# Optimization experiments

Hardware: AMD Instinct MI355X
Metric: run time of the kernel (lower is better)

The kernel has to match this reference:

```python
import jax, jax.numpy as jnp
import numpy as np

N_NODES = 100000


def gcn_conv(x, src, dst, w, W, b, n):
    # PyG GCNConv: add self loops (weight 1), symmetric normalization,
    # linear transform, scatter-add aggregation, bias.
    loop = jnp.arange(n, dtype=src.dtype)
    s = jnp.concatenate([src, loop])
    d = jnp.concatenate([dst, loop])
    ew = jnp.concatenate([w, jnp.ones((n,), dtype=w.dtype)])
    deg = jax.ops.segment_sum(ew, d, num_segments=n)          # [N]
    dinv = jnp.where(deg > 0, jax.lax.rsqrt(deg), 0.0).astype(x.dtype)
    norm = dinv[s] * ew * dinv[d]                             # [E+N]
    h = x @ W                                                 # [N, out]
    msg = h[s] * norm[:, None]                                # gather + scale
    out = jax.ops.segment_sum(msg, d, num_segments=n)         # scatter-add
    return out + b


def setup_inputs() -> dict:
    key = jax.random.key(0)
    k1, k2, k3, k4, k5, k6 = jax.random.split(key, 6)
    n, e, c_in, c_hid, c_out = N_NODES, 1200000, 64, 64, 32
    node_matrix = jax.random.normal(k1, (n, c_in), dtype=jnp.float32)
    edge_index = jax.random.randint(k2, (2, e), 0, n, dtype=jnp.int64)
    edge_weights = jax.random.uniform(k3, (e,), dtype=jnp.float32)
    s_in = 1.0 / np.sqrt(c_in)
    s_hid = 1.0 / np.sqrt(c_hid)
    W1 = jax.random.uniform(k4, (c_in, c_hid), jnp.float32, -s_in, s_in)
    b1 = jnp.zeros((c_hid,), jnp.float32)
    W2 = jax.random.uniform(k5, (c_hid, c_out), jnp.float32, -s_hid, s_hid)
    b2 = jnp.zeros((c_out,), jnp.float32)
    return {"node_matrix": node_matrix, "edge_index": edge_index,
            "edge_weights": edge_weights, "W1": W1, "b1": b1, "W2": W2, "b2": b2}


def reference(node_matrix, edge_index, edge_weights, W1, b1, W2, b2):
    n = node_matrix.shape[0]
    src, dst = edge_index[0], edge_index[1]
    x = gcn_conv(node_matrix, src, dst, edge_weights, W1, b1, n)
    x = jax.nn.relu(x)
    x = gcn_conv(x, src, dst, edge_weights, W2, b2, n)
    return x
```

## Files before the change

kernel.cpp:

```cpp
#include <hip/hip_runtime.h>

static inline int ceil_div(long long a, long long b) { return (int)((a + b - 1) / b); }

#define RBITS 8
#define RNODES 256
#define CAPB 12
#define CAP 4096

typedef __attribute__((ext_vector_type(8))) short bf16x8;
typedef __attribute__((ext_vector_type(4))) float f32x4;
typedef __attribute__((ext_vector_type(2))) unsigned u32x2;
typedef __attribute__((ext_vector_type(4))) unsigned u32x4;

__device__ inline unsigned f2bf(float f) {
    unsigned u = __float_as_uint(f);
    return (u + 0x7fffu + ((u >> 16) & 1u)) >> 16;
}
__device__ inline unsigned pack2(float a, float b) { return f2bf(a) | (f2bf(b) << 16); }
__device__ inline float bf2f(unsigned v) { return __uint_as_float(v << 16); }
__device__ inline float bf_lo(unsigned v) { return __uint_as_float(v << 16); }
__device__ inline float bf_hi(unsigned v) { return __uint_as_float(v & 0xffff0000u); }

#define SC_T 512
#define SC_K 8
#define SC_E (SC_T * SC_K)
__global__ void bin_scatter(const int* __restrict__ src, const int* __restrict__ dst,
                            const float* __restrict__ w, int* __restrict__ bin_cursor,
                            int* __restrict__ bp, float* __restrict__ bw,
                            int NB, int E) {
    __shared__ int hist[512];
    __shared__ int offs[512];
    __shared__ int base[512];
    __shared__ int stage_p[SC_E];
    __shared__ float stage_w[SC_E];
    __shared__ unsigned short stage_b[SC_E];
    int t = threadIdx.x;
    hist[t] = 0;
    __syncthreads();
    int e0 = blockIdx.x * SC_E;
    int nE = E - e0; if (nE > SC_E) nE = SC_E;

    int myBin[SC_K], myRank[SC_K], myPack[SC_K];
    float myW[SC_K];
#pragma unroll
    for (int k = 0; k < SC_K; ++k) {
        int idx = t + k * SC_T;
        if (idx < nE) {
            int e = e0 + idx;
            int d = dst[e];
            int b = d >> RBITS;
            myBin[k] = b;
            myPack[k] = (src[e] << RBITS) | (d & (RNODES - 1));
            myW[k] = w[e];
            myRank[k] = atomicAdd(&hist[b], 1);
        }
    }
    __syncthreads();
    offs[t] = hist[t];
    __syncthreads();
    for (int d = 1; d < 512; d <<= 1) {
        int a = (t >= d) ? offs[t - d] : 0;
        __syncthreads();
        offs[t] += a;
        __syncthreads();
    }
    if (t < NB && hist[t]) base[t] = (t << CAPB) + atomicAdd(&bin_cursor[t], hist[t]);
#pragma unroll
    for (int k = 0; k < SC_K; ++k) {
        int idx = t + k * SC_T;
        if (idx < nE) {
            int b = myBin[k];
            int pos = (offs[b] - hist[b]) + myRank[k];
            stage_p[pos] = myPack[k];
            stage_w[pos] = myW[k];
            stage_b[pos] = (unsigned short)b;
        }
    }
    __syncthreads();
    for (int p = t; p < nE; p += SC_T) {
        int b = stage_b[p];
        int g = base[b] + (p - (offs[b] - hist[b]));
        bp[g] = stage_p[p];
        bw[g] = stage_w[p];
    }
}

__global__ void build_csr(const int* __restrict__ bp, const float* __restrict__ bw,
                          const int* __restrict__ bin_len,
                          unsigned* __restrict__ row_rc, float* __restrict__ dinv,
                          u32x2* __restrict__ ew, int N) {
    __shared__ int bp_s[CAP];
    __shared__ float bw_s[CAP];
    __shared__ int cnt[RNODES];
    __shared__ float wsum[RNODES];
    __shared__ int starts[RNODES];
    __shared__ int cur[RNODES];
    int b = blockIdx.x;
    int t = threadIdx.x;
    int len = bin_len[b];
    int base = b << CAPB;
    if (t < RNODES) { cnt[t] = 0; wsum[t] = 0.f; }
    __syncthreads();
    for (int e = t; e < len; e += 512) {
        int p = bp[base + e];
        float wv = bw[base + e];
        bp_s[e] = p;
        bw_s[e] = wv;
        atomicAdd(&cnt[p & (RNODES - 1)], 1);
        atomicAdd(&wsum[p & (RNODES - 1)], wv);
    }
    __syncthreads();
    if (t < RNODES) starts[t] = cnt[t];
    __syncthreads();
    for (int d = 1; d < RNODES; d <<= 1) {
        int a = 0;
        if (t < RNODES && t >= d) a = starts[t - d];
        __syncthreads();
        if (t < RNODES) starts[t] += a;
        __syncthreads();
    }
    if (t < RNODES) {
        int s0 = starts[t] - cnt[t];
        cur[t] = s0;
        int node = (b << RBITS) + t;
        if (node < N) {
            row_rc[node] = (unsigned)(base + s0) | ((unsigned)cnt[t] << 21);
            dinv[node] = rsqrtf(wsum[t] + 1.0f);
        }
    }
    __syncthreads();
    for (int e = t; e < len; e += 512) {
        int p = bp_s[e];
        int slot = atomicAdd(&cur[p & (RNODES - 1)], 1);
        u32x2 v;
        v.x = (unsigned)(p >> RBITS);
        v.y = __float_as_uint(bw_s[e]);
        ew[base + slot] = v;
    }
}

__global__ __launch_bounds__(256) void gemm1_mfma(const float* __restrict__ X,
                                                  const float* __restrict__ W,
                                                  const float* __restrict__ dinv,
                                                  unsigned short* __restrict__ H, int N) {
    int lane = threadIdx.x & 63;
    int wv = threadIdx.x >> 6;
    int quad = lane >> 4;
    int col = lane & 15;

    bf16x8 Bh[4][2], Bl[4][2];
#pragma unroll
    for (int nt = 0; nt < 4; ++nt)
#pragma unroll
        for (int kh = 0; kh < 2; ++kh)
#pragma unroll
            for (int j = 0; j < 8; ++j) {
                float wval = W[(kh * 32 + quad * 8 + j) * 64 + nt * 16 + col];
                unsigned hb = f2bf(wval);
                Bh[nt][kh][j] = (short)hb;
                Bl[nt][kh][j] = (short)f2bf(wval - bf2f(hb));
            }

#pragma unroll
    for (int rt = 0; rt < 4; ++rt) {
        int rb = blockIdx.x * 256 + wv * 64 + rt * 16;
        if (rb >= N) break;
        int arow = rb + col;
        bf16x8 Ah[2], Al[2];
#pragma unroll
        for (int kh = 0; kh < 2; ++kh) {
            float xv[8];
            if (arow < N) {
                const float4* p = (const float4*)(X + (size_t)arow * 64 + kh * 32 + quad * 8);
                float4 f0 = p[0], f1 = p[1];
                xv[0] = f0.x; xv[1] = f0.y; xv[2] = f0.z; xv[3] = f0.w;
                xv[4] = f1.x; xv[5] = f1.y; xv[6] = f1.z; xv[7] = f1.w;
            } else {
#pragma unroll
                for (int j = 0; j < 8; ++j) xv[j] = 0.f;
            }
#pragma unroll
            for (int j = 0; j < 8; ++j) {
                unsigned hb = f2bf(xv[j]);
                Ah[kh][j] = (short)hb;
                Al[kh][j] = (short)f2bf(xv[j] - bf2f(hb));
            }
        }
        f32x4 acc[4] = {{0,0,0,0},{0,0,0,0},{0,0,0,0},{0,0,0,0}};
#pragma unroll
        for (int nt = 0; nt < 4; ++nt)
#pragma unroll
            for (int kh = 0; kh < 2; ++kh) {
                acc[nt] = __builtin_amdgcn_mfma_f32_16x16x32_bf16(Ah[kh], Bh[nt][kh], acc[nt], 0, 0, 0);
                acc[nt] = __builtin_amdgcn_mfma_f32_16x16x32_bf16(Al[kh], Bh[nt][kh], acc[nt], 0, 0, 0);
                acc[nt] = __builtin_amdgcn_mfma_f32_16x16x32_bf16(Ah[kh], Bl[nt][kh], acc[nt], 0, 0, 0);
            }
        float di[4];
#pragma unroll
        for (int r = 0; r < 4; ++r) {
            int row = rb + quad * 4 + r;
            di[r] = (row < N) ? dinv[row] : 0.f;
        }
#pragma unroll
        for (int nt = 0; nt < 4; ++nt)
#pragma unroll
            for (int r = 0; r < 4; ++r) {
                int row = rb + quad * 4 + r;
                if (row < N)
                    H[(size_t)row * 64 + nt * 16 + col] = (unsigned short)f2bf(di[r] * acc[nt][r]);
            }
    }
}

__global__ __launch_bounds__(256) void gemm2_mfma(const unsigned short* __restrict__ Xb,
                                                  const float* __restrict__ W,
                                                  const float* __restrict__ dinv,
                                                  unsigned short* __restrict__ H, int N) {
    int lane = threadIdx.x & 63;
    int wv = threadIdx.x >> 6;
    int quad = lane >> 4;
    int col = lane & 15;

    bf16x8 Bh[2][2], Bl[2][2];
#pragma unroll
    for (int nt = 0; nt < 2; ++nt)
#pragma unroll
        for (int kh = 0; kh < 2; ++kh)
#pragma unroll
            for (int j = 0; j < 8; ++j) {
                float wval = W[(kh * 32 + quad * 8 + j) * 32 + nt * 16 + col];
                unsigned hb = f2bf(wval);
                Bh[nt][kh][j] = (short)hb;
                Bl[nt][kh][j] = (short)f2bf(wval - bf2f(hb));
            }

#pragma unroll
    for (int rt = 0; rt < 4; ++rt) {
        int rb = blockIdx.x * 256 + wv * 64 + rt * 16;
        if (rb >= N) break;
        int arow = rb + col;
        bf16x8 A[2];
#pragma unroll
        for (int kh = 0; kh < 2; ++kh) {
            if (arow < N) {
                const bf16x8* p = (const bf16x8*)(Xb + (size_t)arow * 64 + kh * 32 + quad * 8);
                A[kh] = *p;
            } else {
                A[kh] = bf16x8{0,0,0,0,0,0,0,0};
            }
        }
        f32x4 acc[2] = {{0,0,0,0},{0,0,0,0}};
#pragma unroll
        for (int nt = 0; nt < 2; ++nt)
#pragma unroll
            for (int kh = 0; kh < 2; ++kh) {
                acc[nt] = __builtin_amdgcn_mfma_f32_16x16x32_bf16(A[kh], Bh[nt][kh], acc[nt], 0, 0, 0);
                acc[nt] = __builtin_amdgcn_mfma_f32_16x16x32_bf16(A[kh], Bl[nt][kh], acc[nt], 0, 0, 0);
            }
        float di[4];
#pragma unroll
        for (int r = 0; r < 4; ++r) {
            int row = rb + quad * 4 + r;
            di[r] = (row < N) ? dinv[row] : 0.f;
        }
#pragma unroll
        for (int nt = 0; nt < 2; ++nt)
#pragma unroll
            for (int r = 0; r < 4; ++r) {
                int row = rb + quad * 4 + r;
                if (row < N)
                    H[(size_t)row * 32 + nt * 16 + col] = (unsigned short)f2bf(di[r] * acc[nt][r]);
            }
    }
}

__global__ void aggregate64(const unsigned* __restrict__ h, const unsigned* __restrict__ row_rc,
                            const u32x2* __restrict__ ew, const float* __restrict__ dinv,
                            const float* __restrict__ b, unsigned* __restrict__ outb, int N) {
    int t = threadIdx.x;
    int c = t & 7;
    int i = blockIdx.x * 64 + (t >> 3);
    if (i >= N) return;
    unsigned rc = row_rc[i];
    int e = (int)(rc & 0x1FFFFFu);
    int end = e + (int)(rc >> 21);
    const uint4* h4 = (const uint4*)h;
    float acc[8];
#pragma unroll
    for (int j = 0; j < 8; ++j) acc[j] = 0.f;
    for (; e + 3 < end; e += 4) {
        u32x2 e0 = __builtin_nontemporal_load(&ew[e]);
        u32x2 e1 = __builtin_nontemporal_load(&ew[e + 1]);
        u32x2 e2 = __builtin_nontemporal_load(&ew[e + 2]);
        u32x2 e3 = __builtin_nontemporal_load(&ew[e + 3]);
        float n0 = __uint_as_float(e0.y);
        float n1 = __uint_as_float(e1.y);
        float n2 = __uint_as_float(e2.y);
        float n3 = __uint_as_float(e3.y);
        uint4 v0 = h4[(size_t)e0.x * 8 + c];
        uint4 v1 = h4[(size_t)e1.x * 8 + c];
        uint4 v2 = h4[(size_t)e2.x * 8 + c];
        uint4 v3 = h4[(size_t)e3.x * 8 + c];
        acc[0] += n0 * bf_lo(v0.x) + n1 * bf_lo(v1.x) + n2 * bf_lo(v2.x) + n3 * bf_lo(v3.x);
        acc[1] += n0 * bf_hi(v0.x) + n1 * bf_hi(v1.x) + n2 * bf_hi(v2.x) + n3 * bf_hi(v3.x);
        acc[2] += n0 * bf_lo(v0.y) + n1 * bf_lo(v1.y) + n2 * bf_lo(v2.y) + n3 * bf_lo(v3.y);
        acc[3] += n0 * bf_hi(v0.y) + n1 * bf_hi(v1.y) + n2 * bf_hi(v2.y) + n3 * bf_hi(v3.y);
        acc[4] += n0 * bf_lo(v0.z) + n1 * bf_lo(v1.z) + n2 * bf_lo(v2.z) + n3 * bf_lo(v3.z);
        acc[5] += n0 * bf_hi(v0.z) + n1 * bf_hi(v1.z) + n2 * bf_hi(v2.z) + n3 * bf_hi(v3.z);
        acc[6] += n0 * bf_lo(v0.w) + n1 * bf_lo(v1.w) + n2 * bf_lo(v2.w) + n3 * bf_lo(v3.w);
        acc[7] += n0 * bf_hi(v0.w) + n1 * bf_hi(v1.w) + n2 * bf_hi(v2.w) + n3 * bf_hi(v3.w);
    }
    for (; e < end; ++e) {
        u32x2 e0 = __builtin_nontemporal_load(&ew[e]);
        float n0 = __uint_as_float(e0.y);
        uint4 v0 = h4[(size_t)e0.x * 8 + c];
        acc[0] += n0 * bf_lo(v0.x);
        acc[1] += n0 * bf_hi(v0.x);
        acc[2] += n0 * bf_lo(v0.y);
        acc[3] += n0 * bf_hi(v0.y);
        acc[4] += n0 * bf_lo(v0.z);
        acc[5] += n0 * bf_hi(v0.z);
        acc[6] += n0 * bf_lo(v0.w);
        acc[7] += n0 * bf_hi(v0.w);
    }
    float di = dinv[i];
    uint4 hv = h4[(size_t)i * 8 + c];
    float hs[8] = {bf_lo(hv.x), bf_hi(hv.x), bf_lo(hv.y), bf_hi(hv.y),
                   bf_lo(hv.z), bf_hi(hv.z), bf_lo(hv.w), bf_hi(hv.w)};
    float4 b0 = ((const float4*)b)[c * 2];
    float4 b1 = ((const float4*)b)[c * 2 + 1];
    float o[8];
    o[0] = b0.x + di * (hs[0] + acc[0]);
    o[1] = b0.y + di * (hs[1] + acc[1]);
    o[2] = b0.z + di * (hs[2] + acc[2]);
    o[3] = b0.w + di * (hs[3] + acc[3]);
    o[4] = b1.x + di * (hs[4] + acc[4]);
    o[5] = b1.y + di * (hs[5] + acc[5]);
    o[6] = b1.z + di * (hs[6] + acc[6]);
    o[7] = b1.w + di * (hs[7] + acc[7]);
#pragma unroll
    for (int j = 0; j < 8; ++j) o[j] = fmaxf(o[j], 0.f);
    u32x4 ov;
    ov.x = pack2(o[0], o[1]);
    ov.y = pack2(o[2], o[3]);
    ov.z = pack2(o[4], o[5]);
    ov.w = pack2(o[6], o[7]);
    __builtin_nontemporal_store(ov, (u32x4*)outb + (size_t)i * 8 + c);
}

__global__ void aggregate32(const unsigned* __restrict__ h, const unsigned* __restrict__ row_rc,
                            const u32x2* __restrict__ ew, const float* __restrict__ dinv,
                            const float* __restrict__ b, float* __restrict__ out, int N) {
    int t = threadIdx.x;
    int c = t & 3;
    int i = blockIdx.x * 128 + (t >> 2);
    if (i >= N) return;
    unsigned rc = row_rc[i];
    int e = (int)(rc & 0x1FFFFFu);
    int end = e + (int)(rc >> 21);
    const uint4* h4 = (const uint4*)h;
    float acc[8];
#pragma unroll
    for (int j = 0; j < 8; ++j) acc[j] = 0.f;
    for (; e + 3 < end; e += 4) {
        u32x2 e0 = __builtin_nontemporal_load(&ew[e]);
        u32x2 e1 = __builtin_nontemporal_load(&ew[e + 1]);
        u32x2 e2 = __builtin_nontemporal_load(&ew[e + 2]);
        u32x2 e3 = __builtin_nontemporal_load(&ew[e + 3]);
        float n0 = __uint_as_float(e0.y);
        float n1 = __uint_as_float(e1.y);
        float n2 = __uint_as_float(e2.y);
        float n3 = __uint_as_float(e3.y);
        uint4 v0 = h4[(size_t)e0.x * 4 + c];
        uint4 v1 = h4[(size_t)e1.x * 4 + c];
        uint4 v2 = h4[(size_t)e2.x * 4 + c];
        uint4 v3 = h4[(size_t)e3.x * 4 + c];
        acc[0] += n0 * bf_lo(v0.x) + n1 * bf_lo(v1.x) + n2 * bf_lo(v2.x) + n3 * bf_lo(v3.x);
        acc[1] += n0 * bf_hi(v0.x) + n1 * bf_hi(v1.x) + n2 * bf_hi(v2.x) + n3 * bf_hi(v3.x);
        acc[2] += n0 * bf_lo(v0.y) + n1 * bf_lo(v1.y) + n2 * bf_lo(v2.y) + n3 * bf_lo(v3.y);
        acc[3] += n0 * bf_hi(v0.y) + n1 * bf_hi(v1.y) + n2 * bf_hi(v2.y) + n3 * bf_hi(v3.y);
        acc[4] += n0 * bf_lo(v0.z) + n1 * bf_lo(v1.z) + n2 * bf_lo(v2.z) + n3 * bf_lo(v3.z);
        acc[5] += n0 * bf_hi(v0.z) + n1 * bf_hi(v1.z) + n2 * bf_hi(v2.z) + n3 * bf_hi(v3.z);
        acc[6] += n0 * bf_lo(v0.w) + n1 * bf_lo(v1.w) + n2 * bf_lo(v2.w) + n3 * bf_lo(v3.w);
        acc[7] += n0 * bf_hi(v0.w) + n1 * bf_hi(v1.w) + n2 * bf_hi(v2.w) + n3 * bf_hi(v3.w);
    }
    for (; e < end; ++e) {
        u32x2 e0 = __builtin_nontemporal_load(&ew[e]);
        float n0 = __uint_as_float(e0.y);
        uint4 v0 = h4[(size_t)e0.x * 4 + c];
        acc[0] += n0 * bf_lo(v0.x);
        acc[1] += n0 * bf_hi(v0.x);
        acc[2] += n0 * bf_lo(v0.y);
        acc[3] += n0 * bf_hi(v0.y);
        acc[4] += n0 * bf_lo(v0.z);
        acc[5] += n0 * bf_hi(v0.z);
        acc[6] += n0 * bf_lo(v0.w);
        acc[7] += n0 * bf_hi(v0.w);
    }
    float di = dinv[i];
    uint4 hv = h4[(size_t)i * 4 + c];
    float hs[8] = {bf_lo(hv.x), bf_hi(hv.x), bf_lo(hv.y), bf_hi(hv.y),
                   bf_lo(hv.z), bf_hi(hv.z), bf_lo(hv.w), bf_hi(hv.w)};
    float4 b0 = ((const float4*)b)[c * 2];
    float4 b1 = ((const float4*)b)[c * 2 + 1];
    f32x4 o0, o1;
    o0.x = b0.x + di * (hs[0] + acc[0]);
    o0.y = b0.y + di * (hs[1] + acc[1]);
    o0.z = b0.z + di * (hs[2] + acc[2]);
    o0.w = b0.w + di * (hs[3] + acc[3]);
    o1.x = b1.x + di * (hs[4] + acc[4]);
    o1.y = b1.y + di * (hs[5] + acc[5]);
    o1.z = b1.z + di * (hs[6] + acc[6]);
    o1.w = b1.w + di * (hs[7] + acc[7]);
    f32x4* op = (f32x4*)(out + (size_t)i * 32 + c * 8);
    __builtin_nontemporal_store(o0, op);
    __builtin_nontemporal_store(o1, op + 1);
}

extern "C" void kernel_launch(void* const* d_in, const int* in_sizes, int n_in,
                              void* d_out, int out_size, void* d_ws, size_t ws_size,
                              hipStream_t stream) {
    const float* x  = (const float*)d_in[0];
    const int* eidx = (const int*)d_in[1];
    const float* w  = (const float*)d_in[2];
    const float* W1 = (const float*)d_in[3];
    const float* b1 = (const float*)d_in[4];
    const float* W2 = (const float*)d_in[5];
    const float* b2 = (const float*)d_in[6];
    float* out = (float*)d_out;

    const int E = in_sizes[2];
    const int N = in_sizes[0] / 64;
    const int* src = eidx;
    const int* dst = eidx + E;
    const int NB = ceil_div(N, RNODES);

    char* ws = (char*)d_ws;
    size_t off = 0;
    auto alloc = [&](size_t bytes) -> void* {
        void* p = ws + off;
        off = (off + bytes + 255) & ~(size_t)255;
        return p;
    };
    int*      bin_cursor = (int*)alloc((size_t)NB * 4);
    int*      bp         = (int*)alloc((size_t)NB * CAP * 4);
    float*    bw         = (float*)alloc((size_t)NB * CAP * 4);
    u32x2*    ew         = (u32x2*)alloc((size_t)NB * CAP * 8);
    unsigned* row_rc     = (unsigned*)alloc((size_t)N * 4);
    float*    dinv       = (float*)alloc((size_t)N * 4);
    unsigned* h1         = (unsigned*)alloc((size_t)N * 32 * 4);
    unsigned* out1b      = (unsigned*)alloc((size_t)N * 32 * 4);
    unsigned* h2         = (unsigned*)alloc((size_t)N * 16 * 4);

    (void)hipMemsetAsync(bin_cursor, 0, (size_t)NB * 4, stream);
    bin_scatter<<<ceil_div(E, SC_E), SC_T, 0, stream>>>(src, dst, w, bin_cursor, bp, bw, NB, E);
    build_csr<<<NB, 512, 0, stream>>>(bp, bw, bin_cursor, row_rc, dinv, ew, N);

    gemm1_mfma<<<ceil_div(N, 256), 256, 0, stream>>>(x, W1, dinv, (unsigned short*)h1, N);
    aggregate64<<<ceil_div(N, 64), 512, 0, stream>>>(h1, row_rc, ew, dinv, b1, out1b, N);

    gemm2_mfma<<<ceil_div(N, 256), 256, 0, stream>>>((const unsigned short*)out1b, W2, dinv,
                                                     (unsigned short*)h2, N);
    aggregate32<<<ceil_div(N, 128), 512, 0, stream>>>(h2, row_rc, ew, dinv, b2, out, N);
}
```

Before: 213.0 us.

## Split each node's edges across four teams, shrink GEMM blocks, defer rsqrt

The aggregation kernels now give each node four teams of lanes. Each team takes a contiguous slice of the node's edge list, and the partial sums are combined with xor shuffles. This targets long per-node serial loops and uneven degree latency. Both GEMM kernels now process one 16-row tile per wave with four times more blocks, and dinv is recomputed from a stored weight sum instead of being precomputed. Nontemporal loads and stores were also replaced with plain accesses. In exchange the code does more shuffle work, and three of every four lanes sit idle in the epilogue.

```diff
diff --git a/kernel.cpp b/kernel.cpp
--- a/kernel.cpp
+++ b/kernel.cpp
@@ -30,7 +30,7 @@
                             int NB, int E) {
     __shared__ int hist[512];
     __shared__ int offs[512];
-    __shared__ int base[512];
+    __shared__ int basex[512];
     __shared__ int stage_p[SC_E];
     __shared__ float stage_w[SC_E];
     __shared__ unsigned short stage_b[SC_E];
@@ -64,7 +64,7 @@
         offs[t] += a;
         __syncthreads();
     }
-    if (t < NB && hist[t]) base[t] = (t << CAPB) + atomicAdd(&bin_cursor[t], hist[t]);
+    if (t < NB && hist[t]) basex[t] = (t << CAPB) + atomicAdd(&bin_cursor[t], hist[t]);
 #pragma unroll
     for (int k = 0; k < SC_K; ++k) {
         int idx = t + k * SC_T;
@@ -79,7 +79,7 @@
     __syncthreads();
     for (int p = t; p < nE; p += SC_T) {
         int b = stage_b[p];
-        int g = base[b] + (p - (offs[b] - hist[b]));
+        int g = basex[b] + (p - (offs[b] - hist[b]));
         bp[g] = stage_p[p];
         bw[g] = stage_w[p];
     }
@@ -87,7 +87,7 @@
 
 __global__ void build_csr(const int* __restrict__ bp, const float* __restrict__ bw,
                           const int* __restrict__ bin_len,
-                          unsigned* __restrict__ row_rc, float* __restrict__ dinv,
+                          unsigned* __restrict__ row_rc, float* __restrict__ wsum_g,
                           u32x2* __restrict__ ew, int N) {
     __shared__ int bp_s[CAP];
     __shared__ float bw_s[CAP];
@@ -125,7 +125,7 @@
         int node = (b << RBITS) + t;
         if (node < N) {
             row_rc[node] = (unsigned)(base + s0) | ((unsigned)cnt[t] << 21);
-            dinv[node] = rsqrtf(wsum[t] + 1.0f);
+            wsum_g[node] = wsum[t];
         }
     }
     __syncthreads();
@@ -141,12 +141,14 @@
 
 __global__ __launch_bounds__(256) void gemm1_mfma(const float* __restrict__ X,
                                                   const float* __restrict__ W,
-                                                  const float* __restrict__ dinv,
+                                                  const float* __restrict__ wsum,
                                                   unsigned short* __restrict__ H, int N) {
     int lane = threadIdx.x & 63;
     int wv = threadIdx.x >> 6;
     int quad = lane >> 4;
     int col = lane & 15;
+    int rb = blockIdx.x * 64 + wv * 16;
+    if (rb >= N) return;
 
     bf16x8 Bh[4][2], Bl[4][2];
 #pragma unroll
@@ -161,65 +163,62 @@
                 Bl[nt][kh][j] = (short)f2bf(wval - bf2f(hb));
             }
 
-#pragma unroll
-    for (int rt = 0; rt < 4; ++rt) {
-        int rb = blockIdx.x * 256 + wv * 64 + rt * 16;
-        if (rb >= N) break;
-        int arow = rb + col;
-        bf16x8 Ah[2], Al[2];
+    int arow = rb + col;
+    bf16x8 Ah[2], Al[2];
+#pragma unroll
+    for (int kh = 0; kh < 2; ++kh) {
+        float xv[8];
+        if (arow < N) {
+            const float4* p = (const float4*)(X + (size_t)arow * 64 + kh * 32 + quad * 8);
+            float4 f0 = p[0], f1 = p[1];
+            xv[0] = f0.x; xv[1] = f0.y; xv[2] = f0.z; xv[3] = f0.w;
+            xv[4] = f1.x; xv[5] = f1.y; xv[6] = f1.z; xv[7] = f1.w;
+        } else {
+#pragma unroll
+            for (int j = 0; j < 8; ++j) xv[j] = 0.f;
+        }
+#pragma unroll
+        for (int j = 0; j < 8; ++j) {
+            unsigned hb = f2bf(xv[j]);
+            Ah[kh][j] = (short)hb;
+            Al[kh][j] = (short)f2bf(xv[j] - bf2f(hb));
+        }
+    }
+    f32x4 acc[4] = {{0,0,0,0},{0,0,0,0},{0,0,0,0},{0,0,0,0}};
+#pragma unroll
+    for (int nt = 0; nt < 4; ++nt)
 #pragma unroll
         for (int kh = 0; kh < 2; ++kh) {
-            float xv[8];
-            if (arow < N) {
-                const float4* p = (const float4*)(X + (size_t)arow * 64 + kh * 32 + quad * 8);
-                float4 f0 = p[0], f1 = p[1];
-                xv[0] = f0.x; xv[1] = f0.y; xv[2] = f0.z; xv[3] = f0.w;
-                xv[4] = f1.x; xv[5] = f1.y; xv[6] = f1.z; xv[7] = f1.w;
-            } else {
-#pragma unroll
-                for (int j = 0; j < 8; ++j) xv[j] = 0.f;
-            }
-#pragma unroll
-            for (int j = 0; j < 8; ++j) {
-                unsigned hb = f2bf(xv[j]);
-                Ah[kh][j] = (short)hb;
-                Al[kh][j] = (short)f2bf(xv[j] - bf2f(hb));
-            }
-        }
-        f32x4 acc[4] = {{0,0,0,0},{0,0,0,0},{0,0,0,0},{0,0,0,0}};
-#pragma unroll
-        for (int nt = 0; nt < 4; ++nt)
-#pragma unroll
-            for (int kh = 0; kh < 2; ++kh) {
-                acc[nt] = __builtin_amdgcn_mfma_f32_16x16x32_bf16(Ah[kh], Bh[nt][kh], acc[nt], 0, 0, 0);
-                acc[nt] = __builtin_amdgcn_mfma_f32_16x16x32_bf16(Al[kh], Bh[nt][kh], acc[nt], 0, 0, 0);
-                acc[nt] = __builtin_amdgcn_mfma_f32_16x16x32_bf16(Ah[kh], Bl[nt][kh], acc[nt], 0, 0, 0);
-            }
-        float di[4];
+            acc[nt] = __builtin_amdgcn_mfma_f32_16x16x32_bf16(Ah[kh], Bh[nt][kh], acc[nt], 0, 0, 0);
+            acc[nt] = __builtin_amdgcn_mfma_f32_16x16x32_bf16(Al[kh], Bh[nt][kh], acc[nt], 0, 0, 0);
+            acc[nt] = __builtin_amdgcn_mfma_f32_16x16x32_bf16(Ah[kh], Bl[nt][kh], acc[nt], 0, 0, 0);
+        }
+    float di[4];
+#pragma unroll
+    for (int r = 0; r < 4; ++r) {
+        int row = rb + quad * 4 + r;
+        di[r] = (row < N) ? rsqrtf(wsum[row] + 1.0f) : 0.f;
+    }
+#pragma unroll
+    for (int nt = 0; nt < 4; ++nt)
 #pragma unroll
         for (int r = 0; r < 4; ++r) {
             int row = rb + quad * 4 + r;
-            di[r] = (row < N) ? dinv[row] : 0.f;
-        }
-#pragma unroll
-        for (int nt = 0; nt < 4; ++nt)
-#pragma unroll
-            for (int r = 0; r < 4; ++r) {
-                int row = rb + quad * 4 + r;
-                if (row < N)
-                    H[(size_t)row * 64 + nt * 16 + col] = (unsigned short)f2bf(di[r] * acc[nt][r]);
-            }
-    }
+            if (row < N)
+                H[(size_t)row * 64 + nt * 16 + col] = (unsigned short)f2bf(di[r] * acc[nt][r]);
+        }
 }
 
 __global__ __launch_bounds__(256) void gemm2_mfma(const unsigned short* __restrict__ Xb,
                                                   const float* __restrict__ W,
-                                                  const float* __restrict__ dinv,
+                                                  const float* __restrict__ wsum,
                                                   unsigned short* __restrict__ H, int N) {
     int lane = threadIdx.x & 63;
     int wv = threadIdx.x >> 6;
     int quad = lane >> 4;
     int col = lane & 15;
+    int rb = blockIdx.x * 64 + wv * 16;
+    if (rb >= N) return;
 
     bf16x8 Bh[2][2], Bl[2][2];
 #pragma unroll
@@ -234,65 +233,63 @@
                 Bl[nt][kh][j] = (short)f2bf(wval - bf2f(hb));
             }
 
-#pragma unroll
-    for (int rt = 0; rt < 4; ++rt) {
-        int rb = blockIdx.x * 256 + wv * 64 + rt * 16;
-        if (rb >= N) break;
-        int arow = rb + col;
-        bf16x8 A[2];
+    int arow = rb + col;
+    bf16x8 A[2];
+#pragma unroll
+    for (int kh = 0; kh < 2; ++kh) {
+        if (arow < N) {
+            const bf16x8* p = (const bf16x8*)(Xb + (size_t)arow * 64 + kh * 32 + quad * 8);
+            A[kh] = *p;
+        } else {
+            A[kh] = bf16x8{0,0,0,0,0,0,0,0};
+        }
+    }
+    f32x4 acc[2] = {{0,0,0,0},{0,0,0,0}};
+#pragma unroll
+    for (int nt = 0; nt < 2; ++nt)
 #pragma unroll
         for (int kh = 0; kh < 2; ++kh) {
-            if (arow < N) {
-                const bf16x8* p = (const bf16x8*)(Xb + (size_t)arow * 64 + kh * 32 + quad * 8);
-                A[kh] = *p;
-            } else {
-                A[kh] = bf16x8{0,0,0,0,0,0,0,0};
-            }
-        }
-        f32x4 acc[2] = {{0,0,0,0},{0,0,0,0}};
-#pragma unroll
-        for (int nt = 0; nt < 2; ++nt)
-#pragma unroll
-            for (int kh = 0; kh < 2; ++kh) {
-                acc[nt] = __builtin_amdgcn_mfma_f32_16x16x32_bf16(A[kh], Bh[nt][kh], acc[nt], 0, 0, 0);
-                acc[nt] = __builtin_amdgcn_mfma_f32_16x16x32_bf16(A[kh], Bl[nt][kh], acc[nt], 0, 0, 0);
-            }
-        float di[4];
+            acc[nt] = __builtin_amdgcn_mfma_f32_16x16x32_bf16(A[kh], Bh[nt][kh], acc[nt], 0, 0, 0);
+            acc[nt] = __builtin_amdgcn_mfma_f32_16x16x32_bf16(A[kh], Bl[nt][kh], acc[nt], 0, 0, 0);
+        }
+    float di[4];
+#pragma unroll
+    for (int r = 0; r < 4; ++r) {
+        int row = rb + quad * 4 + r;
+        di[r] = (row < N) ? rsqrtf(wsum[row] + 1.0f) : 0.f;
+    }
+#pragma unroll
+    for (int nt = 0; nt < 2; ++nt)
 #pragma unroll
         for (int r = 0; r < 4; ++r) {
             int row = rb + quad * 4 + r;
-            di[r] = (row < N) ? dinv[row] : 0.f;
-        }
-#pragma unroll
-        for (int nt = 0; nt < 2; ++nt)
-#pragma unroll
-            for (int r = 0; r < 4; ++r) {
-                int row = rb + quad * 4 + r;
-                if (row < N)
-                    H[(size_t)row * 32 + nt * 16 + col] = (unsigned short)f2bf(di[r] * acc[nt][r]);
-            }
-    }
+            if (row < N)
+                H[(size_t)row * 32 + nt * 16 + col] = (unsigned short)f2bf(di[r] * acc[nt][r]);
+        }
 }
 
 __global__ void aggregate64(const unsigned* __restrict__ h, const unsigned* __restrict__ row_rc,
-                            const u32x2* __restrict__ ew, const float* __restrict__ dinv,
+                            const u32x2* __restrict__ ew, const float* __restrict__ wsum,
                             const float* __restrict__ b, unsigned* __restrict__ outb, int N) {
     int t = threadIdx.x;
     int c = t & 7;
-    int i = blockIdx.x * 64 + (t >> 3);
+    int team = (t >> 3) & 3;
+    int i = blockIdx.x * 16 + (t >> 5);
     if (i >= N) return;
     unsigned rc = row_rc[i];
-    int e = (int)(rc & 0x1FFFFFu);
-    int end = e + (int)(rc >> 21);
+    int beg = (int)(rc & 0x1FFFFFu);
+    int len = (int)(rc >> 21);
+    int q = len >> 2, r = len & 3;
+    int myCnt = q + (team < r ? 1 : 0);
+    int myBeg = beg + team * q + (team < r ? team : r);
     const uint4* h4 = (const uint4*)h;
     float acc[8];
 #pragma unroll
     for (int j = 0; j < 8; ++j) acc[j] = 0.f;
-    for (; e + 3 < end; e += 4) {
-        u32x2 e0 = __builtin_nontemporal_load(&ew[e]);
-        u32x2 e1 = __builtin_nontemporal_load(&ew[e + 1]);
-        u32x2 e2 = __builtin_nontemporal_load(&ew[e + 2]);
-        u32x2 e3 = __builtin_nontemporal_load(&ew[e + 3]);
+    int k = 0;
+    for (; k + 3 < myCnt; k += 4) {
+        int e = myBeg + k;
+        u32x2 e0 = ew[e], e1 = ew[e + 1], e2 = ew[e + 2], e3 = ew[e + 3];
         float n0 = __uint_as_float(e0.y);
         float n1 = __uint_as_float(e1.y);
         float n2 = __uint_as_float(e2.y);
@@ -310,8 +307,9 @@
         acc[6] += n0 * bf_lo(v0.w) + n1 * bf_lo(v1.w) + n2 * bf_lo(v2.w) + n3 * bf_lo(v3.w);
         acc[7] += n0 * bf_hi(v0.w) + n1 * bf_hi(v1.w) + n2 * bf_hi(v2.w) + n3 * bf_hi(v3.w);
     }
-    for (; e < end; ++e) {
-        u32x2 e0 = __builtin_nontemporal_load(&ew[e]);
+    for (; k < myCnt; ++k) {
+        int e = myBeg + k;
+        u32x2 e0 = ew[e];
         float n0 = __uint_as_float(e0.y);
         uint4 v0 = h4[(size_t)e0.x * 8 + c];
         acc[0] += n0 * bf_lo(v0.x);
@@ -323,7 +321,12 @@
         acc[6] += n0 * bf_lo(v0.w);
         acc[7] += n0 * bf_hi(v0.w);
     }
-    float di = dinv[i];
+#pragma unroll
+    for (int j = 0; j < 8; ++j) acc[j] += __shfl_xor(acc[j], 8, 64);
+#pragma unroll
+    for (int j = 0; j < 8; ++j) acc[j] += __shfl_xor(acc[j], 16, 64);
+    if (team != 0) return;
+    float di = rsqrtf(wsum[i] + 1.0f);
     uint4 hv = h4[(size_t)i * 8 + c];
     float hs[8] = {bf_lo(hv.x), bf_hi(hv.x), bf_lo(hv.y), bf_hi(hv.y),
                    bf_lo(hv.z), bf_hi(hv.z), bf_lo(hv.w), bf_hi(hv.w)};
@@ -340,33 +343,36 @@
     o[7] = b1.w + di * (hs[7] + acc[7]);
 #pragma unroll
     for (int j = 0; j < 8; ++j) o[j] = fmaxf(o[j], 0.f);
-    u32x4 ov;
+    uint4 ov;
     ov.x = pack2(o[0], o[1]);
     ov.y = pack2(o[2], o[3]);
     ov.z = pack2(o[4], o[5]);
     ov.w = pack2(o[6], o[7]);
-    __builtin_nontemporal_store(ov, (u32x4*)outb + (size_t)i * 8 + c);
+    ((uint4*)outb)[(size_t)i * 8 + c] = ov;
 }
 
 __global__ void aggregate32(const unsigned* __restrict__ h, const unsigned* __restrict__ row_rc,
-                            const u32x2* __restrict__ ew, const float* __restrict__ dinv,
+                            const u32x2* __restrict__ ew, const float* __restrict__ wsum,
                             const float* __restrict__ b, float* __restrict__ out, int N) {
     int t = threadIdx.x;
     int c = t & 3;
-    int i = blockIdx.x * 128 + (t >> 2);
+    int team = (t >> 2) & 3;
+    int i = blockIdx.x * 32 + (t >> 4);
     if (i >= N) return;
     unsigned rc = row_rc[i];
-    int e = (int)(rc & 0x1FFFFFu);
-    int end = e + (int)(rc >> 21);
+    int beg = (int)(rc & 0x1FFFFFu);
+    int len = (int)(rc >> 21);
+    int q = len >> 2, r = len & 3;
+    int myCnt = q + (team < r ? 1 : 0);
+    int myBeg = beg + team * q + (team < r ? team : r);
     const uint4* h4 = (const uint4*)h;
     float acc[8];
 #pragma unroll
     for (int j = 0; j < 8; ++j) acc[j] = 0.f;
-    for (; e + 3 < end; e += 4) {
-        u32x2 e0 = __builtin_nontemporal_load(&ew[e]);
-        u32x2 e1 = __builtin_nontemporal_load(&ew[e + 1]);
-        u32x2 e2 = __builtin_nontemporal_load(&ew[e + 2]);
-        u32x2 e3 = __builtin_nontemporal_load(&ew[e + 3]);
+    int k = 0;
+    for (; k + 3 < myCnt; k += 4) {
+        int e = myBeg + k;
+        u32x2 e0 = ew[e], e1 = ew[e + 1], e2 = ew[e + 2], e3 = ew[e + 3];
         float n0 = __uint_as_float(e0.y);
         float n1 = __uint_as_float(e1.y);
         float n2 = __uint_as_float(e2.y);
@@ -384,8 +390,9 @@
         acc[6] += n0 * bf_lo(v0.w) + n1 * bf_lo(v1.w) + n2 * bf_lo(v2.w) + n3 * bf_lo(v3.w);
         acc[7] += n0 * bf_hi(v0.w) + n1 * bf_hi(v1.w) + n2 * bf_hi(v2.w) + n3 * bf_hi(v3.w);
     }
-    for (; e < end; ++e) {
-        u32x2 e0 = __builtin_nontemporal_load(&ew[e]);
+    for (; k < myCnt; ++k) {
+        int e = myBeg + k;
+        u32x2 e0 = ew[e];
         float n0 = __uint_as_float(e0.y);
         uint4 v0 = h4[(size_t)e0.x * 4 + c];
         acc[0] += n0 * bf_lo(v0.x);
@@ -397,7 +404,12 @@
         acc[6] += n0 * bf_lo(v0.w);
         acc[7] += n0 * bf_hi(v0.w);
     }
-    float di = dinv[i];
+#pragma unroll
+    for (int j = 0; j < 8; ++j) acc[j] += __shfl_xor(acc[j], 4, 64);
+#pragma unroll
+    for (int j = 0; j < 8; ++j) acc[j] += __shfl_xor(acc[j], 8, 64);
+    if (team != 0) return;
+    float di = rsqrtf(wsum[i] + 1.0f);
     uint4 hv = h4[(size_t)i * 4 + c];
     float hs[8] = {bf_lo(hv.x), bf_hi(hv.x), bf_lo(hv.y), bf_hi(hv.y),
                    bf_lo(hv.z), bf_hi(hv.z), bf_lo(hv.w), bf_hi(hv.w)};
@@ -447,19 +459,19 @@
     float*    bw         = (float*)alloc((size_t)NB * CAP * 4);
     u32x2*    ew         = (u32x2*)alloc((size_t)NB * CAP * 8);
     unsigned* row_rc     = (unsigned*)alloc((size_t)N * 4);
-    float*    dinv       = (float*)alloc((size_t)N * 4);
+    float*    wsum       = (float*)alloc((size_t)N * 4);
     unsigned* h1         = (unsigned*)alloc((size_t)N * 32 * 4);
     unsigned* out1b      = (unsigned*)alloc((size_t)N * 32 * 4);
     unsigned* h2         = (unsigned*)alloc((size_t)N * 16 * 4);
 
     (void)hipMemsetAsync(bin_cursor, 0, (size_t)NB * 4, stream);
     bin_scatter<<<ceil_div(E, SC_E), SC_T, 0, stream>>>(src, dst, w, bin_cursor, bp, bw, NB, E);
-    build_csr<<<NB, 512, 0, stream>>>(bp, bw, bin_cursor, row_rc, dinv, ew, N);
-
-    gemm1_mfma<<<ceil_div(N, 256), 256, 0, stream>>>(x, W1, dinv, (unsigned short*)h1, N);
-    aggregate64<<<ceil_div(N, 64), 512, 0, stream>>>(h1, row_rc, ew, dinv, b1, out1b, N);
-
-    gemm2_mfma<<<ceil_div(N, 256), 256, 0, stream>>>((const unsigned short*)out1b, W2, dinv,
-                                                     (unsigned short*)h2, N);
-    aggregate32<<<ceil_div(N, 128), 512, 0, stream>>>(h2, row_rc, ew, dinv, b2, out, N);
-}
+    build_csr<<<NB, 512, 0, stream>>>(bp, bw, bin_cursor, row_rc, wsum, ew, N);
+
+    gemm1_mfma<<<ceil_div(N, 64), 256, 0, stream>>>(x, W1, wsum, (unsigned short*)h1, N);
+    aggregate64<<<ceil_div(N, 16), 512, 0, stream>>>(h1, row_rc, ew, wsum, b1, out1b, N);
+
+    gemm2_mfma<<<ceil_div(N, 64), 256, 0, stream>>>((const unsigned short*)out1b, W2, wsum,
+                                                    (unsigned short*)h2, N);
+    aggregate32<<<ceil_div(N, 32), 512, 0, stream>>>(h2, row_rc, ew, wsum, b2, out, N);
+}
```

After: 196.0 us. 1.09x faster.
